# Kernel optimization log

Hardware: AMD Instinct MI355X
Metric: run time of the kernel (lower is better)

Reference implementation:

```python
import jax, jax.numpy as jnp
import numpy as np

C_RGLRU = 8.0

def _rg_lru(x, wa, ba, wx, bx, lam):
    # x: [B, L, D]. Griffin RG-LRU (De et al. 2024).
    r = jax.nn.sigmoid(jnp.einsum('bld,ed->ble', x, wa) + ba)
    i = jax.nn.sigmoid(jnp.einsum('bld,ed->ble', x, wx) + bx)
    log_a = -C_RGLRU * r * jax.nn.softplus(lam)          # [B,L,D], <= 0
    a = jnp.exp(log_a)
    mult = jnp.sqrt(jnp.maximum(1.0 - jnp.exp(2.0 * log_a), 0.0))
    b = mult * (i * x)
    def combine(c1, c2):
        a1, b1 = c1
        a2, b2 = c2
        return a1 * a2, a2 * b1 + b2
    _, h = jax.lax.associative_scan(combine, (a, b), axis=1)
    return h

def setup_inputs() -> dict:
    key = jax.random.key(0)
    ks = jax.random.split(key, 12)
    B, L, D, R = 4, 2048, 2048, 2560
    s_d = 1.0 / np.sqrt(D)
    s_r = 1.0 / np.sqrt(R)
    s_c = 1.0 / np.sqrt(R * 4)
    return {
        'x':      jax.random.normal(ks[0], (B, L, D), jnp.float32),
        'w1':     jax.random.normal(ks[1], (R, D), jnp.float32) * s_d,
        'b1':     jnp.zeros((R,), jnp.float32),
        'conv_w': jax.random.normal(ks[2], (R, R, 4), jnp.float32) * s_c,
        'conv_b': jnp.zeros((R,), jnp.float32),
        'wa':     jax.random.normal(ks[3], (R, R), jnp.float32) * s_r,
        'ba':     jnp.zeros((R,), jnp.float32),
        'wx':     jax.random.normal(ks[4], (R, R), jnp.float32) * s_r,
        'bx':     jnp.zeros((R,), jnp.float32),
        'lam':    jax.random.uniform(ks[5], (R,), jnp.float32, 0.5, 2.0),
        'w2':     jax.random.normal(ks[6], (D, R), jnp.float32) * s_r,
        'b2':     jnp.zeros((D,), jnp.float32),
    }

def reference(x, w1, b1, conv_w, conv_b, wa, ba, wx, bx, lam, w2, b2):
    # linear1 + SiLU: [B,L,D] -> [B,L,R]
    h = jax.nn.silu(jnp.einsum('bld,rd->blr', x, w1) + b1)
    # temporal conv1d: kernel 4, dilation 2, padding 3 both sides (as in torch)
    hc = h.transpose(0, 2, 1)  # [B,R,L]
    hc = jax.lax.conv_general_dilated(
        hc, conv_w, window_strides=(1,), padding=[(3, 3)],
        rhs_dilation=(2,), dimension_numbers=('NCH', 'OIH', 'NCH'))
    hc = hc + conv_b[None, :, None]
    h = hc.transpose(0, 2, 1)  # [B,L,R]
    # RG-LRU gated linear recurrence
    h = _rg_lru(h, wa, ba, wx, bx, lam)
    # linear2: [B,L,R] -> [B,L,D]
    return jnp.einsum('blr,dr->bld', h, w2) + b2
```

## Files before the change

kernel.cpp:

```cpp
#include <hip/hip_runtime.h>

#define B_  4
#define L_  2048
#define D_  2048
#define R_  2560
#define BL_ (B_ * L_)
#define LP_ (L_ + 6)

#define CHK_  16
#define CLEN_ (L_ / CHK_)

typedef unsigned short u16;
typedef unsigned int   u32;

typedef __attribute__((ext_vector_type(8))) short short8;
typedef __attribute__((ext_vector_type(4))) float f32x4;

static __device__ __forceinline__ u16 f2bf(float f) {
  u32 x = __float_as_uint(f);
  x += 0x7fffu + ((x >> 16) & 1u);
  return (u16)(x >> 16);
}
static __device__ __forceinline__ float bf2f(u16 u) {
  return __uint_as_float(((u32)u) << 16);
}

static __device__ __forceinline__ void gld16(const u16* g, u16* l) {
  __builtin_amdgcn_global_load_lds(
      (const __attribute__((address_space(1))) void*)g,
      (__attribute__((address_space(3))) void*)l, 16, 0, 0);
}

#define SB0()     __builtin_amdgcn_sched_barrier(0)
#define BAR()     __builtin_amdgcn_s_barrier()
#define LGKM0()   do { asm volatile("s_waitcnt lgkmcnt(0)" ::: "memory"); SB0(); } while (0)

__global__ void cvt_bf16(const float* __restrict__ src, u16* __restrict__ dst, int n) {
  int i = blockIdx.x * blockDim.x + threadIdx.x;
  int stride = gridDim.x * blockDim.x;
  for (; i < n; i += stride) dst[i] = f2bf(src[i]);
}

__global__ void cvt_convw(const float* __restrict__ cw, u16* __restrict__ out) {
  int i = blockIdx.x * blockDim.x + threadIdx.x;
  if (i >= R_ * R_) return;
  const float4 v = *(const float4*)(cw + (size_t)i * 4);
  out[(size_t)0 * R_ * R_ + i] = f2bf(v.x);
  out[(size_t)1 * R_ * R_ + i] = f2bf(v.y);
  out[(size_t)2 * R_ * R_ + i] = f2bf(v.z);
  out[(size_t)3 * R_ * R_ + i] = f2bf(v.w);
}

__global__ void zero_pads(u16* __restrict__ h1p) {
  int i = blockIdx.x * blockDim.x + threadIdx.x;
  if (i >= 24 * R_) return;
  const int rr = i / R_, c = i % R_;
  const int b = rr / 6, k = rr % 6;
  const int row = b * LP_ + (k < 3 ? k : L_ + k);
  h1p[(size_t)row * R_ + c] = 0;
}

template <int NF, int IB>
__device__ __forceinline__ void mfma_block(f32x4 (&acc)[8][NF], const short8 (&aF)[4],
                                           const short8 (&bF)[NF]) {
#pragma unroll
  for (int i = 0; i < 4; ++i)
#pragma unroll
    for (int j = 0; j < NF; ++j)
      acc[IB + i][j] =
          __builtin_amdgcn_mfma_f32_16x16x32_bf16(aF[i], bF[j], acc[IB + i][j], 0, 0, 0);
}

template <int KDIM, int TAPS, int NF, int ACT, int OBF16, int PADOUT>
__global__ __launch_bounds__(512)
__attribute__((amdgpu_waves_per_eu(2, 2)))
void gemm256(const u16* __restrict__ A, const u16* __restrict__ Bm,
             const float* __restrict__ bias, void* __restrict__ Cv, int N) {
  constexpr int NTK = KDIM / 64;
  constexpr int NT  = NTK * TAPS;
  constexpr int BN  = NF * 64;
  constexpr int BUFU16 = 16384 + NF * 4096;
  __shared__ u16 lds[2][BUFU16];

  const int tid  = threadIdx.x;
  const int wave = tid >> 6, lane = tid & 63;
  const int wr = wave >> 2, wc = wave & 3;
  const int q = lane >> 4, r16 = lane & 15;
  const int rsw = r16 & 7;
  const int bm = blockIdx.x * 256, bn = blockIdx.y * BN;
  const int srow = tid >> 3;
  const int schunk = (tid & 7) ^ (srow & 7);
  const int bbatch = bm >> 11;
  const int arow0 = (TAPS == 4) ? (bm + 3 + 6 * bbatch) : bm;

  f32x4 acc[8][NF] = {};

  auto stA = [&](int u, int h) {
    const int uc = (u < NT) ? u : (NT - 1);
    const int tap = uc / NTK;
    const int ku  = (uc % NTK) * 64;
    const int sh  = (TAPS == 4) ? (2 * tap - 3) : 0;
    const u16* src = A + (size_t)(arow0 + sh + h * 128) * KDIM + ku + schunk * 8;
    u16* dst = &lds[u & 1][h * 8192 + wave * 512];
#pragma unroll
    for (int s = 0; s < 2; ++s)
      gld16(src + (size_t)(s * 64 + srow) * KDIM, dst + s * 4096);
  };
  auto stB = [&](int u, int j) {
    const int uc = (u < NT) ? u : (NT - 1);
    const int tap = uc / NTK;
    const int ku  = (uc % NTK) * 64;
    const u16* src = Bm + (size_t)tap * R_ * R_ +
                     (size_t)(bn + j * 64 + srow) * KDIM + ku + schunk * 8;
    gld16(src, &lds[u & 1][16384 + j * 4096 + wave * 512]);
  };
  auto ldA = [&](short8 (&f)[4], int p, int half, int k) {
    const int base = half * 8192 + (wr * 64 + r16) * 64 + ((k * 4 + q) ^ rsw) * 8;
#pragma unroll
    for (int i = 0; i < 4; ++i)
      f[i] = *(const short8*)&lds[p][base + i * 1024];
  };
  auto ldB = [&](short8 (&f)[NF], int p, int k) {
    const int base = 16384 + (wc * 16 + r16) * 64 + ((k * 4 + q) ^ rsw) * 8;
#pragma unroll
    for (int j = 0; j < NF; ++j)
      f[j] = *(const short8*)&lds[p][base + j * 4096];
  };

  stA(0, 0); stA(0, 1);
#pragma unroll
  for (int j = 0; j < NF; ++j) stB(0, j);
  stA(1, 0);
#pragma unroll
  for (int j = 0; j < NF; ++j) stB(1, j);
  asm volatile("s_waitcnt vmcnt(%0)" :: "n"(NF + 2) : "memory");
  SB0();
  BAR();

  short8 aF[4], bF[NF];
  for (int t = 0; t < NT; ++t) {
    const int p = t & 1;
    ldA(aF, p, 0, 0);
    ldB(bF, p, 0);
    stA(t + 1, 1);
    BAR(); LGKM0();
    __builtin_amdgcn_s_setprio(1);
    mfma_block<NF, 0>(acc, aF, bF);
    __builtin_amdgcn_s_setprio(0);
    SB0(); BAR();
    ldA(aF, p, 1, 0);
    BAR(); LGKM0();
    __builtin_amdgcn_s_setprio(1);
    mfma_block<NF, 4>(acc, aF, bF);
    __builtin_amdgcn_s_setprio(0);
    SB0(); BAR();
    ldA(aF, p, 0, 1);
    ldB(bF, p, 1);
    BAR(); LGKM0();
    __builtin_amdgcn_s_setprio(1);
    mfma_block<NF, 0>(acc, aF, bF);
    __builtin_amdgcn_s_setprio(0);
    SB0(); BAR();
    ldA(aF, p, 1, 1);
    stA(t + 2, 0);
#pragma unroll
    for (int j = 0; j < NF; ++j) stB(t + 2, j);
    BAR(); LGKM0();
    __builtin_amdgcn_s_setprio(1);
    mfma_block<NF, 4>(acc, aF, bF);
    __builtin_amdgcn_s_setprio(0);
    asm volatile("s_waitcnt vmcnt(%0)" :: "n"(NF + 2) : "memory");
    SB0(); BAR();
  }

#pragma unroll
  for (int i = 0; i < 8; ++i) {
    const int rb  = ((i & 4) ? 128 : 0) + wr * 64 + (i & 3) * 16;
    const int row = bm + rb + q * 4;
    const int orow = PADOUT ? (row + 3 + 6 * bbatch) : row;
#pragma unroll
    for (int j = 0; j < NF; ++j) {
      const int col = bn + j * 64 + wc * 16 + r16;
      const float bv = bias[col];
#pragma unroll
      for (int rr = 0; rr < 4; ++rr) {
        float v = acc[i][j][rr] + bv;
        if (ACT == 1) v = v / (1.f + __expf(-v));
        const size_t off = (size_t)(orow + rr) * N + col;
        if (OBF16) ((u16*)Cv)[off] = f2bf(v);
        else       ((float*)Cv)[off] = v;
      }
    }
  }
}

__global__ void gate_ew(const u16* __restrict__ gab, const u16* __restrict__ gib,
                        const u16* __restrict__ h2b, const float* __restrict__ lam,
                        float* __restrict__ a32, float* __restrict__ b32) {
  int idx = blockIdx.x * blockDim.x + threadIdx.x;
  if (idx >= BL_ * R_) return;
  const int r = idx % R_;
  const float ga = bf2f(gab[idx]);
  const float gi = bf2f(gib[idx]);
  const float h2 = bf2f(h2b[idx]);
  const float rr = 1.f / (1.f + __expf(-ga));
  const float ii = 1.f / (1.f + __expf(-gi));
  const float lm = lam[r];
  const float sp = log1pf(__expf(lm));
  const float log_a = -8.f * rr * sp;
  const float a  = __expf(log_a);
  const float e2 = __expf(2.f * log_a);
  const float mult = sqrtf(fmaxf(1.f - e2, 0.f));
  a32[idx] = a;
  b32[idx] = mult * ii * h2;
}

__global__ void scan_pass1(const float* __restrict__ a32, const float* __restrict__ b32,
                           float* __restrict__ Aprod, float* __restrict__ Hend) {
  int t = blockIdx.x * blockDim.x + threadIdx.x;
  if (t >= CHK_ * B_ * R_) return;
  const int c = t / (B_ * R_), br = t % (B_ * R_);
  const int b = br / R_, r = br % R_;
  size_t idx = ((size_t)b * L_ + c * CLEN_) * R_ + r;
  float Ap = 1.f, h = 0.f;
  for (int l = 0; l < CLEN_; ++l) {
    const float a = a32[idx], bb = b32[idx];
    Ap *= a;
    h = a * h + bb;
    idx += R_;
  }
  Aprod[t] = Ap;
  Hend[t]  = h;
}

__global__ void scan_pass2(const float* __restrict__ Aprod, float* __restrict__ Hend) {
  int br = blockIdx.x * blockDim.x + threadIdx.x;
  if (br >= B_ * R_) return;
  float h = Hend[br];
  for (int c = 1; c < CHK_; ++c) {
    const int i = c * (B_ * R_) + br;
    h = Hend[i] + Aprod[i] * h;
    Hend[i] = h;
  }
}

__global__ void scan_pass3(const float* __restrict__ a32, const float* __restrict__ b32,
                           const float* __restrict__ Hend, u16* __restrict__ hs) {
  int t = blockIdx.x * blockDim.x + threadIdx.x;
  if (t >= CHK_ * B_ * R_) return;
  const int c = t / (B_ * R_), br = t % (B_ * R_);
  const int b = br / R_, r = br % R_;
  float h = (c == 0) ? 0.f : Hend[(size_t)(c - 1) * (B_ * R_) + br];
  size_t idx = ((size_t)b * L_ + c * CLEN_) * R_ + r;
  for (int l = 0; l < CLEN_; ++l) {
    h = a32[idx] * h + b32[idx];
    hs[idx] = f2bf(h);
    idx += R_;
  }
}

extern "C" void kernel_launch(void* const* d_in, const int* in_sizes, int n_in,
                              void* d_out, int out_size, void* d_ws, size_t ws_size,
                              hipStream_t stream) {
  (void)in_sizes; (void)n_in; (void)out_size; (void)ws_size;
  const float* x   = (const float*)d_in[0];
  const float* w1  = (const float*)d_in[1];
  const float* b1  = (const float*)d_in[2];
  const float* cw  = (const float*)d_in[3];
  const float* cb  = (const float*)d_in[4];
  const float* wa  = (const float*)d_in[5];
  const float* ba  = (const float*)d_in[6];
  const float* wx  = (const float*)d_in[7];
  const float* bx  = (const float*)d_in[8];
  const float* lam = (const float*)d_in[9];
  const float* w2  = (const float*)d_in[10];
  const float* b2  = (const float*)d_in[11];

  char* ws = (char*)d_ws;
  size_t o = 0;
  auto alloc = [&](size_t bytes) { char* p = ws + o; o += (bytes + 255) & ~255ull; return p; };

  u16* w2b = (u16*)alloc((size_t)D_ * R_ * 2);
  u16* wab = (u16*)alloc((size_t)R_ * R_ * 2);
  u16* wxb = (u16*)alloc((size_t)R_ * R_ * 2);
  char* a32p = ws + o;
  u16* xb  = (u16*)alloc((size_t)BL_ * D_ * 2);
  u16* w1b = (u16*)alloc((size_t)R_ * D_ * 2);
  u16* cwb = (u16*)alloc((size_t)4 * R_ * R_ * 2);
  char* b32p = ws + o;
  u16* h1p = (u16*)alloc((size_t)B_ * LP_ * R_ * 2);
  alloc((size_t)BL_ * R_ * 4 - (size_t)B_ * LP_ * R_ * 2);
  u16* h2b = (u16*)alloc((size_t)BL_ * R_ * 2);
  u16* gab = (u16*)alloc((size_t)BL_ * R_ * 2);
  u16* gib = (u16*)alloc((size_t)BL_ * R_ * 2);
  float* Aprod = (float*)alloc((size_t)CHK_ * B_ * R_ * 4);
  float* Hend  = (float*)alloc((size_t)CHK_ * B_ * R_ * 4);
  float* a32 = (float*)a32p;
  float* b32 = (float*)b32p;
  u16* hsb = gab;

  cvt_bf16<<<4096, 256, 0, stream>>>(x,  xb,  BL_ * D_);
  cvt_bf16<<<2048, 256, 0, stream>>>(w1, w1b, R_ * D_);
  cvt_bf16<<<2048, 256, 0, stream>>>(wa, wab, R_ * R_);
  cvt_bf16<<<2048, 256, 0, stream>>>(wx, wxb, R_ * R_);
  cvt_bf16<<<2048, 256, 0, stream>>>(w2, w2b, D_ * R_);
  cvt_convw<<<(R_ * R_ + 255) / 256, 256, 0, stream>>>(cw, cwb);
  zero_pads<<<(24 * R_ + 255) / 256, 256, 0, stream>>>(h1p);

  gemm256<2048, 1, 5, 1, 1, 1><<<dim3(32, 8), 512, 0, stream>>>(xb, w1b, b1, h1p, R_);
  gemm256<2560, 4, 5, 0, 1, 0><<<dim3(32, 8), 512, 0, stream>>>(h1p, cwb, cb, h2b, R_);
  gemm256<2560, 1, 5, 0, 1, 0><<<dim3(32, 8), 512, 0, stream>>>(h2b, wab, ba, gab, R_);
  gemm256<2560, 1, 5, 0, 1, 0><<<dim3(32, 8), 512, 0, stream>>>(h2b, wxb, bx, gib, R_);
  gate_ew<<<(BL_ * R_ + 255) / 256, 256, 0, stream>>>(gab, gib, h2b, lam, a32, b32);
  scan_pass1<<<(CHK_ * B_ * R_ + 255) / 256, 256, 0, stream>>>(a32, b32, Aprod, Hend);
  scan_pass2<<<(B_ * R_ + 255) / 256, 256, 0, stream>>>(Aprod, Hend);
  scan_pass3<<<(CHK_ * B_ * R_ + 255) / 256, 256, 0, stream>>>(a32, b32, Hend, hsb);
  gemm256<2560, 1, 4, 0, 0, 0><<<dim3(32, 8), 512, 0, stream>>>(hsb, w2b, b2, d_out, D_);
}
```

Measured before the change: 1.618 ms.

## Double-buffer GEMM register fragments to overlap LDS reads with MFMA

The GEMM main loop now keeps two sets of register fragments. It issues the LDS reads for the next sub-block before running the MFMA block on the current one, and prefetches the first fragment of the next tile at the end of each iteration. This is meant to hide LDS read latency behind matrix-core work and to remove some barriers per iteration. In exchange it uses more VGPRs, which may lower occupancy, and it changes the vmcnt wait points, so the ordering is delicate.

```diff
diff --git a/kernel.cpp b/kernel.cpp
--- a/kernel.cpp
+++ b/kernel.cpp
@@ -137,40 +137,50 @@
   SB0();
   BAR();
 
-  short8 aF[4], bF[NF];
+  short8 aX[4], aY[4], bX[NF], bY[NF];
+  ldA(aX, 0, 0, 0);
+  ldB(bX, 0, 0);
+  SB0();
+
+#pragma unroll 1
   for (int t = 0; t < NT; ++t) {
     const int p = t & 1;
-    ldA(aF, p, 0, 0);
-    ldB(bF, p, 0);
+    BAR(); LGKM0();
+    ldA(aY, p, 1, 0);
+    SB0();
+    __builtin_amdgcn_s_setprio(1);
+    mfma_block<NF, 0>(acc, aX, bX);
+    __builtin_amdgcn_s_setprio(0);
     stA(t + 1, 1);
+    SB0();
     BAR(); LGKM0();
+    ldA(aX, p, 0, 1);
+    ldB(bY, p, 1);
+    SB0();
     __builtin_amdgcn_s_setprio(1);
-    mfma_block<NF, 0>(acc, aF, bF);
+    mfma_block<NF, 4>(acc, aY, bX);
     __builtin_amdgcn_s_setprio(0);
-    SB0(); BAR();
-    ldA(aF, p, 1, 0);
+    SB0();
     BAR(); LGKM0();
+    ldA(aY, p, 1, 1);
+    SB0();
     __builtin_amdgcn_s_setprio(1);
-    mfma_block<NF, 4>(acc, aF, bF);
+    mfma_block<NF, 0>(acc, aX, bY);
     __builtin_amdgcn_s_setprio(0);
-    SB0(); BAR();
-    ldA(aF, p, 0, 1);
-    ldB(bF, p, 1);
+    asm volatile("s_waitcnt vmcnt(2)" ::: "memory");
+    SB0();
     BAR(); LGKM0();
+    ldA(aX, p ^ 1, 0, 0);
+    ldB(bX, p ^ 1, 0);
+    SB0();
     __builtin_amdgcn_s_setprio(1);
-    mfma_block<NF, 0>(acc, aF, bF);
+    mfma_block<NF, 4>(acc, aY, bY);
     __builtin_amdgcn_s_setprio(0);
-    SB0(); BAR();
-    ldA(aF, p, 1, 1);
     stA(t + 2, 0);
 #pragma unroll
     for (int j = 0; j < NF; ++j) stB(t + 2, j);
-    BAR(); LGKM0();
-    __builtin_amdgcn_s_setprio(1);
-    mfma_block<NF, 4>(acc, aF, bF);
-    __builtin_amdgcn_s_setprio(0);
     asm volatile("s_waitcnt vmcnt(%0)" :: "n"(NF + 2) : "memory");
-    SB0(); BAR();
+    SB0();
   }
 
 #pragma unroll
```

After: 6.273 ms. 3.88x slower.

## Fuse gate GEMMs, fold gate math into scan, remap GEMM tiles per XCD

Applied to the files above, without the earlier changes.

Concatenates the wa and wx weights so both gate projections run as one GEMM with N=2R, writing a combined bf16 gate buffer. Removes the separate elementwise gate kernel and the fp32 a/b intermediates by recomputing the gate math inside both scan passes. GEMMs switch from a 2D grid with 320-wide tiles to a 1D grid of 256x256 tiles, with a block-index remap that groups tiles by XCD for L2 locality. The trade-off is that the gate math runs twice and the scans now do strided bf16 reads over the wider concatenated buffer.

```diff
diff --git a/kernel.cpp b/kernel.cpp
--- a/kernel.cpp
+++ b/kernel.cpp
@@ -60,6 +60,13 @@
   h1p[(size_t)row * R_ + c] = 0;
 }
 
+__global__ void cat_bias(const float* __restrict__ ba, const float* __restrict__ bx,
+                         float* __restrict__ bcat) {
+  int i = blockIdx.x * blockDim.x + threadIdx.x;
+  if (i < R_) bcat[i] = ba[i];
+  else if (i < 2 * R_) bcat[i] = bx[i - R_];
+}
+
 template <int NF, int IB>
 __device__ __forceinline__ void mfma_block(f32x4 (&acc)[8][NF], const short8 (&aF)[4],
                                            const short8 (&bF)[NF]) {
@@ -71,23 +78,28 @@
           __builtin_amdgcn_mfma_f32_16x16x32_bf16(aF[i], bF[j], acc[IB + i][j], 0, 0, 0);
 }
 
-template <int KDIM, int TAPS, int NF, int ACT, int OBF16, int PADOUT>
+template <int KDIM, int TAPS, int ACT, int OBF16, int PADOUT>
 __global__ __launch_bounds__(512)
 __attribute__((amdgpu_waves_per_eu(2, 2)))
 void gemm256(const u16* __restrict__ A, const u16* __restrict__ Bm,
-             const float* __restrict__ bias, void* __restrict__ Cv, int N) {
+             const float* __restrict__ bias, void* __restrict__ Cv, int N, int NBX) {
+  constexpr int NF  = 4;
   constexpr int NTK = KDIM / 64;
   constexpr int NT  = NTK * TAPS;
-  constexpr int BN  = NF * 64;
   constexpr int BUFU16 = 16384 + NF * 4096;
   __shared__ u16 lds[2][BUFU16];
+
+  const int cpx = gridDim.x >> 3;
+  int lin = blockIdx.x;
+  lin = (lin & 7) * cpx + (lin >> 3);
+  const int bx = lin % NBX, by = lin / NBX;
 
   const int tid  = threadIdx.x;
   const int wave = tid >> 6, lane = tid & 63;
   const int wr = wave >> 2, wc = wave & 3;
   const int q = lane >> 4, r16 = lane & 15;
   const int rsw = r16 & 7;
-  const int bm = blockIdx.x * 256, bn = blockIdx.y * BN;
+  const int bm = bx * 256, bn = by * 256;
   const int srow = tid >> 3;
   const int schunk = (tid & 7) ^ (srow & 7);
   const int bbatch = bm >> 11;
@@ -194,40 +206,38 @@
   }
 }
 
-__global__ void gate_ew(const u16* __restrict__ gab, const u16* __restrict__ gib,
-                        const u16* __restrict__ h2b, const float* __restrict__ lam,
-                        float* __restrict__ a32, float* __restrict__ b32) {
-  int idx = blockIdx.x * blockDim.x + threadIdx.x;
-  if (idx >= BL_ * R_) return;
-  const int r = idx % R_;
-  const float ga = bf2f(gab[idx]);
-  const float gi = bf2f(gib[idx]);
-  const float h2 = bf2f(h2b[idx]);
+static __device__ __forceinline__ void gate_math(u16 ga_, u16 gi_, u16 h2_, float sp,
+                                                 float& a, float& b) {
+  const float ga = bf2f(ga_);
+  const float gi = bf2f(gi_);
+  const float h2 = bf2f(h2_);
   const float rr = 1.f / (1.f + __expf(-ga));
   const float ii = 1.f / (1.f + __expf(-gi));
-  const float lm = lam[r];
-  const float sp = log1pf(__expf(lm));
   const float log_a = -8.f * rr * sp;
-  const float a  = __expf(log_a);
+  a = __expf(log_a);
   const float e2 = __expf(2.f * log_a);
-  const float mult = sqrtf(fmaxf(1.f - e2, 0.f));
-  a32[idx] = a;
-  b32[idx] = mult * ii * h2;
-}
-
-__global__ void scan_pass1(const float* __restrict__ a32, const float* __restrict__ b32,
+  b = sqrtf(fmaxf(1.f - e2, 0.f)) * ii * h2;
+}
+
+__global__ void scan_pass1(const u16* __restrict__ gcat, const u16* __restrict__ h2b,
+                           const float* __restrict__ lam,
                            float* __restrict__ Aprod, float* __restrict__ Hend) {
   int t = blockIdx.x * blockDim.x + threadIdx.x;
   if (t >= CHK_ * B_ * R_) return;
   const int c = t / (B_ * R_), br = t % (B_ * R_);
   const int b = br / R_, r = br % R_;
-  size_t idx = ((size_t)b * L_ + c * CLEN_) * R_ + r;
+  const float sp = log1pf(__expf(lam[r]));
+  size_t rowbase = (size_t)b * L_ + (size_t)c * CLEN_;
+  const u16* pg  = gcat + rowbase * (2 * R_) + r;
+  const u16* ph2 = h2b + rowbase * R_ + r;
   float Ap = 1.f, h = 0.f;
   for (int l = 0; l < CLEN_; ++l) {
-    const float a = a32[idx], bb = b32[idx];
+    float a, bb;
+    gate_math(pg[0], pg[R_], ph2[0], sp, a, bb);
     Ap *= a;
     h = a * h + bb;
-    idx += R_;
+    pg += 2 * R_;
+    ph2 += R_;
   }
   Aprod[t] = Ap;
   Hend[t]  = h;
@@ -244,18 +254,27 @@
   }
 }
 
-__global__ void scan_pass3(const float* __restrict__ a32, const float* __restrict__ b32,
+__global__ void scan_pass3(const u16* __restrict__ gcat, const u16* __restrict__ h2b,
+                           const float* __restrict__ lam,
                            const float* __restrict__ Hend, u16* __restrict__ hs) {
   int t = blockIdx.x * blockDim.x + threadIdx.x;
   if (t >= CHK_ * B_ * R_) return;
   const int c = t / (B_ * R_), br = t % (B_ * R_);
   const int b = br / R_, r = br % R_;
+  const float sp = log1pf(__expf(lam[r]));
   float h = (c == 0) ? 0.f : Hend[(size_t)(c - 1) * (B_ * R_) + br];
-  size_t idx = ((size_t)b * L_ + c * CLEN_) * R_ + r;
+  size_t rowbase = (size_t)b * L_ + (size_t)c * CLEN_;
+  const u16* pg  = gcat + rowbase * (2 * R_) + r;
+  const u16* ph2 = h2b + rowbase * R_ + r;
+  u16* po = hs + rowbase * R_ + r;
   for (int l = 0; l < CLEN_; ++l) {
-    h = a32[idx] * h + b32[idx];
-    hs[idx] = f2bf(h);
-    idx += R_;
+    float a, bb;
+    gate_math(pg[0], pg[R_], ph2[0], sp, a, bb);
+    h = a * h + bb;
+    *po = f2bf(h);
+    pg += 2 * R_;
+    ph2 += R_;
+    po += R_;
   }
 }
 
@@ -280,40 +299,34 @@
   size_t o = 0;
   auto alloc = [&](size_t bytes) { char* p = ws + o; o += (bytes + 255) & ~255ull; return p; };
 
-  u16* w2b = (u16*)alloc((size_t)D_ * R_ * 2);
-  u16* wab = (u16*)alloc((size_t)R_ * R_ * 2);
-  u16* wxb = (u16*)alloc((size_t)R_ * R_ * 2);
-  char* a32p = ws + o;
+  u16* w2b   = (u16*)alloc((size_t)D_ * R_ * 2);
+  u16* wcatb = (u16*)alloc((size_t)2 * R_ * R_ * 2);
+  float* bcat = (float*)alloc((size_t)2 * R_ * 4);
+  char* hsp = ws + o;
   u16* xb  = (u16*)alloc((size_t)BL_ * D_ * 2);
   u16* w1b = (u16*)alloc((size_t)R_ * D_ * 2);
   u16* cwb = (u16*)alloc((size_t)4 * R_ * R_ * 2);
-  char* b32p = ws + o;
   u16* h1p = (u16*)alloc((size_t)B_ * LP_ * R_ * 2);
-  alloc((size_t)BL_ * R_ * 4 - (size_t)B_ * LP_ * R_ * 2);
   u16* h2b = (u16*)alloc((size_t)BL_ * R_ * 2);
-  u16* gab = (u16*)alloc((size_t)BL_ * R_ * 2);
-  u16* gib = (u16*)alloc((size_t)BL_ * R_ * 2);
+  u16* gcat = (u16*)alloc((size_t)BL_ * 2 * R_ * 2);
   float* Aprod = (float*)alloc((size_t)CHK_ * B_ * R_ * 4);
   float* Hend  = (float*)alloc((size_t)CHK_ * B_ * R_ * 4);
-  float* a32 = (float*)a32p;
-  float* b32 = (float*)b32p;
-  u16* hsb = gab;
+  u16* hsb = (u16*)hsp;
 
   cvt_bf16<<<4096, 256, 0, stream>>>(x,  xb,  BL_ * D_);
   cvt_bf16<<<2048, 256, 0, stream>>>(w1, w1b, R_ * D_);
-  cvt_bf16<<<2048, 256, 0, stream>>>(wa, wab, R_ * R_);
-  cvt_bf16<<<2048, 256, 0, stream>>>(wx, wxb, R_ * R_);
+  cvt_bf16<<<2048, 256, 0, stream>>>(wa, wcatb, R_ * R_);
+  cvt_bf16<<<2048, 256, 0, stream>>>(wx, wcatb + (size_t)R_ * R_, R_ * R_);
   cvt_bf16<<<2048, 256, 0, stream>>>(w2, w2b, D_ * R_);
   cvt_convw<<<(R_ * R_ + 255) / 256, 256, 0, stream>>>(cw, cwb);
   zero_pads<<<(24 * R_ + 255) / 256, 256, 0, stream>>>(h1p);
-
-  gemm256<2048, 1, 5, 1, 1, 1><<<dim3(32, 8), 512, 0, stream>>>(xb, w1b, b1, h1p, R_);
-  gemm256<2560, 4, 5, 0, 1, 0><<<dim3(32, 8), 512, 0, stream>>>(h1p, cwb, cb, h2b, R_);
-  gemm256<2560, 1, 5, 0, 1, 0><<<dim3(32, 8), 512, 0, stream>>>(h2b, wab, ba, gab, R_);
-  gemm256<2560, 1, 5, 0, 1, 0><<<dim3(32, 8), 512, 0, stream>>>(h2b, wxb, bx, gib, R_);
-  gate_ew<<<(BL_ * R_ + 255) / 256, 256, 0, stream>>>(gab, gib, h2b, lam, a32, b32);
-  scan_pass1<<<(CHK_ * B_ * R_ + 255) / 256, 256, 0, stream>>>(a32, b32, Aprod, Hend);
+  cat_bias<<<(2 * R_ + 255) / 256, 256, 0, stream>>>(ba, bx, bcat);
+
+  gemm256<2048, 1, 1, 1, 1><<<320, 512, 0, stream>>>(xb, w1b, b1, h1p, R_, 32);
+  gemm256<2560, 4, 0, 1, 0><<<320, 512, 0, stream>>>(h1p, cwb, cb, h2b, R_, 32);
+  gemm256<2560, 1, 0, 1, 0><<<640, 512, 0, stream>>>(h2b, wcatb, bcat, gcat, 2 * R_, 32);
+  scan_pass1<<<(CHK_ * B_ * R_ + 255) / 256, 256, 0, stream>>>(gcat, h2b, lam, Aprod, Hend);
   scan_pass2<<<(B_ * R_ + 255) / 256, 256, 0, stream>>>(Aprod, Hend);
-  scan_pass3<<<(CHK_ * B_ * R_ + 255) / 256, 256, 0, stream>>>(a32, b32, Hend, hsb);
-  gemm256<2560, 1, 4, 0, 0, 0><<<dim3(32, 8), 512, 0, stream>>>(hsb, w2b, b2, d_out, D_);
-}
+  scan_pass3<<<(CHK_ * B_ * R_ + 255) / 256, 256, 0, stream>>>(gcat, h2b, lam, Hend, hsb);
+  gemm256<2560, 1, 0, 0, 0><<<256, 512, 0, stream>>>(hsb, w2b, b2, d_out, D_, 32);
+}
```

Result: faster. 1.347 ms (-16.7%).
